# Optimization experiments

Hardware: AMD Instinct MI355X
Metric: run time of the kernel (lower is better)

Reference implementation:

```python
import jax, jax.numpy as jnp
import numpy as np
from jax import lax

N_IN = 512      # n_input == n_output of decoder
N_H = 2048      # n_hidden
N_L = 2         # n_layers (encoder/decoder GRU stacks written out explicitly)
SEQ = 2048      # sequence length
SPARSITY = 0.1  # sparsity_level -> k_sparse = int(N_H * SPARSITY)


def setup_inputs() -> dict:
    key = jax.random.key(0)
    ks = jax.random.split(key, 14)
    s = 0.02
    f32 = jnp.float32
    return {
        "sequence": jax.random.normal(ks[0], (SEQ, N_IN), f32),
        # encoder GRU (pytorch layout: W_ih [3H, in], W_hh [3H, H], gate order r,z,n)
        "enc_Wih0": jax.random.normal(ks[1], (3 * N_H, N_IN), f32) * s,
        "enc_Wih1": jax.random.normal(ks[2], (3 * N_H, N_H), f32) * s,
        "enc_Whh": jax.random.normal(ks[3], (N_L, 3 * N_H, N_H), f32) * s,
        "enc_bih": jax.random.normal(ks[4], (N_L, 3 * N_H), f32) * s,
        "enc_bhh": jax.random.normal(ks[5], (N_L, 3 * N_H), f32) * s,
        # decoder GRU (input dim = N_IN)
        "dec_Wih0": jax.random.normal(ks[6], (3 * N_H, N_IN), f32) * s,
        "dec_Wih1": jax.random.normal(ks[7], (3 * N_H, N_H), f32) * s,
        "dec_Whh": jax.random.normal(ks[8], (N_L, 3 * N_H, N_H), f32) * s,
        "dec_bih": jax.random.normal(ks[9], (N_L, 3 * N_H), f32) * s,
        "dec_bhh": jax.random.normal(ks[10], (N_L, 3 * N_H), f32) * s,
        # decoder output Linear: n_hidden -> n_output
        "dec_Wout": jax.random.normal(ks[11], (N_IN, N_H), f32) * s,
        "dec_bout": jax.random.normal(ks[12], (N_IN,), f32) * s,
    }


def _gru_cell(x, h, Wih, Whh, bih, bhh):
    # x: [in], h: [H]; PyTorch GRU equations, gate order (r, z, n)
    gi = Wih @ x + bih
    gh = Whh @ h + bhh
    ir, iz, inn = jnp.split(gi, 3)
    hr, hz, hn = jnp.split(gh, 3)
    r = jax.nn.sigmoid(ir + hr)
    z = jax.nn.sigmoid(iz + hz)
    n = jnp.tanh(inn + r * hn)
    return (1.0 - z) * n + z * h


def reference(sequence, enc_Wih0, enc_Wih1, enc_Whh, enc_bih, enc_bhh,
              dec_Wih0, dec_Wih1, dec_Whh, dec_bih, dec_bhh,
              dec_Wout, dec_bout):
    seq_len = sequence.shape[0]

    # ---- encoder: 2-layer GRU over the sequence, batch=1 (batch dim dropped) ----
    def enc_step(h, x):
        h0 = _gru_cell(x, h[0], enc_Wih0, enc_Whh[0], enc_bih[0], enc_bhh[0])
        h1 = _gru_cell(h0, h[1], enc_Wih1, enc_Whh[1], enc_bih[1], enc_bhh[1])
        return jnp.stack([h0, h1]), None

    h0_init = jnp.zeros((N_L, N_H), sequence.dtype)
    enc_hidden, _ = lax.scan(enc_step, h0_init, sequence)

    # ---- top-k sparsity on innermost (last) layer of the hidden state ----
    k_sparse = int(N_H * SPARSITY)
    h_last = enc_hidden[N_L - 1]
    _, top_idx = lax.top_k(h_last, k_sparse)
    mask = jnp.zeros((N_H,), h_last.dtype).at[top_idx].set(1.0)
    enc_hidden = enc_hidden.at[N_L - 1].set(h_last * mask)

    # ---- decoder: seq_len-1 single-step GRU+Linear, targets are sequence reversed ----
    targets = jnp.flip(sequence[: seq_len - 1], axis=0)  # sequence[seq_len-2-i]

    def dec_step(carry, target):
        x, h = carry
        h0 = _gru_cell(x, h[0], dec_Wih0, dec_Whh[0], dec_bih[0], dec_bhh[0])
        h1 = _gru_cell(h0, h[1], dec_Wih1, dec_Whh[1], dec_bih[1], dec_bhh[1])
        out = dec_Wout @ h1 + dec_bout
        step_loss = jnp.mean((out - target) ** 2)
        return (out, jnp.stack([h0, h1])), (out, step_loss)

    init = (sequence[seq_len - 1], enc_hidden)
    _, (reconstructed, step_losses) = lax.scan(dec_step, init, targets)
    loss = jnp.sum(step_losses) / seq_len
    return reconstructed, loss
```

## Files before the change

kernel.cpp:

```cpp
#include <hip/hip_runtime.h>
#include <hip/hip_cooperative_groups.h>

namespace cg = cooperative_groups;

#define H      2048
#define NIN    512
#define TH     (3 * H)
#define SEQLEN 2048
#define KSP    204
#define NBLK   256
#define NTHR   512
#define NWAVES (NBLK * (NTHR / 64))

static_assert(NWAVES == H, "one wave per hidden element");

struct Params {
    const float* seq;
    const float* eWih0; const float* eWih1; const float* eWhh;
    const float* ebih;  const float* ebhh;
    const float* dWih0; const float* dWih1; const float* dWhh;
    const float* dbih;  const float* dbhh;
    const float* dWout; const float* dbout;
    float* out;
    float* ws;
};

__device__ __forceinline__ float wave_reduce_f(float v) {
#pragma unroll
    for (int m = 32; m >= 1; m >>= 1) v += __shfl_xor(v, m, 64);
    return v;
}

template <int XDIM>
__device__ __forceinline__ void gru_phase(int j, int lane,
    const float* __restrict__ Wih, const float* __restrict__ Whh,
    const float* __restrict__ bih, const float* __restrict__ bhh,
    const float* __restrict__ x,
    const float* __restrict__ hcur, float* __restrict__ hnxt)
{
    const float4* wir = (const float4*)(Wih + (size_t)j * XDIM);
    const float4* wiz = (const float4*)(Wih + (size_t)(H + j) * XDIM);
    const float4* win = (const float4*)(Wih + (size_t)(2 * H + j) * XDIM);
    const float4* whr = (const float4*)(Whh + (size_t)j * H);
    const float4* whz = (const float4*)(Whh + (size_t)(H + j) * H);
    const float4* whn = (const float4*)(Whh + (size_t)(2 * H + j) * H);
    const float4* x4  = (const float4*)x;
    const float4* h4  = (const float4*)hcur;

    float air = 0.f, aiz = 0.f, ain = 0.f;
#pragma unroll
    for (int k = 0; k < XDIM / 256; ++k) {
        int i = lane + 64 * k;
        float4 xv = x4[i];
        float4 a = wir[i], b = wiz[i], c = win[i];
        air = fmaf(a.x, xv.x, air); air = fmaf(a.y, xv.y, air);
        air = fmaf(a.z, xv.z, air); air = fmaf(a.w, xv.w, air);
        aiz = fmaf(b.x, xv.x, aiz); aiz = fmaf(b.y, xv.y, aiz);
        aiz = fmaf(b.z, xv.z, aiz); aiz = fmaf(b.w, xv.w, aiz);
        ain = fmaf(c.x, xv.x, ain); ain = fmaf(c.y, xv.y, ain);
        ain = fmaf(c.z, xv.z, ain); ain = fmaf(c.w, xv.w, ain);
    }
    float ahr = 0.f, ahz = 0.f, ahn = 0.f;
#pragma unroll
    for (int k = 0; k < H / 256; ++k) {
        int i = lane + 64 * k;
        float4 hv = h4[i];
        float4 a = whr[i], b = whz[i], c = whn[i];
        ahr = fmaf(a.x, hv.x, ahr); ahr = fmaf(a.y, hv.y, ahr);
        ahr = fmaf(a.z, hv.z, ahr); ahr = fmaf(a.w, hv.w, ahr);
        ahz = fmaf(b.x, hv.x, ahz); ahz = fmaf(b.y, hv.y, ahz);
        ahz = fmaf(b.z, hv.z, ahz); ahz = fmaf(b.w, hv.w, ahz);
        ahn = fmaf(c.x, hv.x, ahn); ahn = fmaf(c.y, hv.y, ahn);
        ahn = fmaf(c.z, hv.z, ahn); ahn = fmaf(c.w, hv.w, ahn);
    }
    float sr   = wave_reduce_f(air + ahr);
    float sz   = wave_reduce_f(aiz + ahz);
    float sin_ = wave_reduce_f(ain);
    float shn  = wave_reduce_f(ahn);

    if (lane == 0) {
        float r = 1.f / (1.f + expf(-(sr + bih[j] + bhh[j])));
        float z = 1.f / (1.f + expf(-(sz + bih[H + j] + bhh[H + j])));
        float n = tanhf(sin_ + bih[2 * H + j] + r * (shn + bhh[2 * H + j]));
        hnxt[j] = (1.f - z) * n + z * hcur[j];
    }
}

__global__ void __launch_bounds__(NTHR)
seqae_kernel(Params p)
{
    cg::grid_group grid = cg::this_grid();
    const int lane = threadIdx.x & 63;
    const int wid  = blockIdx.x * (NTHR / 64) + (threadIdx.x >> 6);

    float* loss = p.ws;
    float* h0a  = p.ws + 64;
    float* h0b  = h0a + H;
    float* h1a  = h0b + H;
    float* h1b  = h1a + H;

    {
        int gtid = blockIdx.x * NTHR + threadIdx.x;
        if (gtid == 0) *loss = 0.f;
        for (int i = gtid; i < H; i += NBLK * NTHR) { h0a[i] = 0.f; h1a[i] = 0.f; }
    }
    grid.sync();

    const float* ebih0 = p.ebih;        const float* ebih1 = p.ebih + TH;
    const float* ebhh0 = p.ebhh;        const float* ebhh1 = p.ebhh + TH;
    const float* eWhh0 = p.eWhh;        const float* eWhh1 = p.eWhh + (size_t)TH * H;

    float* h0c = h0a; float* h0n = h0b;
    float* h1c = h1a; float* h1n = h1b;

    for (int t = 0; t < SEQLEN; ++t) {
        const float* x = p.seq + (size_t)t * NIN;
        gru_phase<NIN>(wid, lane, p.eWih0, eWhh0, ebih0, ebhh0, x, h0c, h0n);
        grid.sync();
        gru_phase<H>(wid, lane, p.eWih1, eWhh1, ebih1, ebhh1, h0n, h1c, h1n);
        grid.sync();
        float* tmp;
        tmp = h0c; h0c = h0n; h0n = tmp;
        tmp = h1c; h1c = h1n; h1n = tmp;
    }

    {
        int j = wid;
        float vj = h1c[j];
        int cnt = 0;
        for (int i = lane; i < H; i += 64) {
            float vi = h1c[i];
            cnt += (vi > vj) || (vi == vj && i < j);
        }
#pragma unroll
        for (int m = 32; m >= 1; m >>= 1) cnt += __shfl_xor(cnt, m, 64);
        if (lane == 0) h1n[j] = (cnt < KSP) ? vj : 0.f;
    }
    grid.sync();
    { float* tmp = h1c; h1c = h1n; h1n = tmp; }

    const float* dbih0 = p.dbih;        const float* dbih1 = p.dbih + TH;
    const float* dbhh0 = p.dbhh;        const float* dbhh1 = p.dbhh + TH;
    const float* dWhh0 = p.dWhh;        const float* dWhh1 = p.dWhh + (size_t)TH * H;

    float lsum = 0.f;
    for (int t = 0; t < SEQLEN - 1; ++t) {
        const float* x = (t == 0) ? (p.seq + (size_t)(SEQLEN - 1) * NIN)
                                  : (p.out + (size_t)(t - 1) * NIN);
        gru_phase<NIN>(wid, lane, p.dWih0, dWhh0, dbih0, dbhh0, x, h0c, h0n);
        grid.sync();
        gru_phase<H>(wid, lane, p.dWih1, dWhh1, dbih1, dbhh1, h0n, h1c, h1n);
        grid.sync();
        if (wid < NIN) {
            int j = wid;
            const float4* wo = (const float4*)(p.dWout + (size_t)j * H);
            const float4* h4 = (const float4*)h1n;
            float a = 0.f;
#pragma unroll
            for (int k = 0; k < H / 256; ++k) {
                int i = lane + 64 * k;
                float4 w = wo[i]; float4 hv = h4[i];
                a = fmaf(w.x, hv.x, a); a = fmaf(w.y, hv.y, a);
                a = fmaf(w.z, hv.z, a); a = fmaf(w.w, hv.w, a);
            }
            a = wave_reduce_f(a);
            if (lane == 0) {
                float o = a + p.dbout[j];
                p.out[(size_t)t * NIN + j] = o;
                float tg = p.seq[(size_t)(SEQLEN - 2 - t) * NIN + j];
                float d = o - tg;
                lsum = fmaf(d, d, lsum);
            }
        }
        grid.sync();
        float* tmp;
        tmp = h0c; h0c = h0n; h0n = tmp;
        tmp = h1c; h1c = h1n; h1n = tmp;
    }

    if (wid < NIN && lane == 0) atomicAdd(loss, lsum);
    grid.sync();
    if (blockIdx.x == 0 && threadIdx.x == 0) {
        p.out[(size_t)(SEQLEN - 1) * NIN] = (*loss) * (1.f / ((float)NIN * (float)SEQLEN));
    }
}

extern "C" void kernel_launch(void* const* d_in, const int* in_sizes, int n_in,
                              void* d_out, int out_size, void* d_ws, size_t ws_size,
                              hipStream_t stream)
{
    Params p;
    p.seq   = (const float*)d_in[0];
    p.eWih0 = (const float*)d_in[1];
    p.eWih1 = (const float*)d_in[2];
    p.eWhh  = (const float*)d_in[3];
    p.ebih  = (const float*)d_in[4];
    p.ebhh  = (const float*)d_in[5];
    p.dWih0 = (const float*)d_in[6];
    p.dWih1 = (const float*)d_in[7];
    p.dWhh  = (const float*)d_in[8];
    p.dbih  = (const float*)d_in[9];
    p.dbhh  = (const float*)d_in[10];
    p.dWout = (const float*)d_in[11];
    p.dbout = (const float*)d_in[12];
    p.out = (float*)d_out;
    p.ws  = (float*)d_ws;

    void* args[] = { &p };
    (void)hipLaunchCooperativeKernel((void*)seqae_kernel, dim3(NBLK), dim3(NTHR),
                                     args, 0, stream);
}
```

Measured before the change: 396.1 ms.

## Keep FP16-packed GRU weights resident in registers and pipeline encoder layers

Adds pack kernels that convert all GRU and output weights to fp16 in a lane-interleaved layout inside the workspace. The main cooperative kernel then keeps each wave's weight rows in registers for the whole encoder or decoder loop, so it no longer re-streams about 100MB of weights from memory every timestep. The encoder also skews layer 1 by one step so both layers run in the same phase, halving the grid syncs per step. The cost is fp16 rounding of the weights, very high register pressure (possible spills), and extra pack launches on every call. A fallback path is kept for when the workspace is too small.

```diff
diff --git a/kernel.cpp b/kernel.cpp
--- a/kernel.cpp
+++ b/kernel.cpp
@@ -1,4 +1,5 @@
 #include <hip/hip_runtime.h>
+#include <hip/hip_fp16.h>
 #include <hip/hip_cooperative_groups.h>
 
 namespace cg = cooperative_groups;
@@ -10,9 +11,20 @@
 #define KSP    204
 #define NBLK   256
 #define NTHR   512
-#define NWAVES (NBLK * (NTHR / 64))
-
-static_assert(NWAVES == H, "one wave per hidden element");
+
+typedef unsigned int uint32;
+
+constexpr long O_EA = 0;
+constexpr long O_EB = O_EA + 1572864;
+constexpr long O_EC = O_EB + 6291456;
+constexpr long O_ED = O_EC + 6291456;
+constexpr long O_DA = O_ED + 6291456;
+constexpr long O_DB = O_DA + 1572864;
+constexpr long O_DC = O_DB + 6291456;
+constexpr long O_DD = O_DC + 6291456;
+constexpr long O_WO = O_DD + 6291456;
+constexpr long U_TOTAL = O_WO + 524288;
+constexpr size_t WS_STATE_BYTES = 65536;
 
 struct Params {
     const float* seq;
@@ -31,8 +43,223 @@
     return v;
 }
 
+__device__ __forceinline__ float sigmoidf_(float v) { return 1.f / (1.f + expf(-v)); }
+
+__device__ __forceinline__ float2 h2f(uint32 u) {
+    __half2 h = *reinterpret_cast<__half2*>(&u);
+    return __half22float2(h);
+}
+
+__global__ void pack_kernel(const float* __restrict__ src, uint32* __restrict__ dst,
+                            int total, int xdim, int nrows)
+{
+    int KK = xdim / 256;
+    for (int i = blockIdx.x * blockDim.x + threadIdx.x; i < total;
+         i += gridDim.x * blockDim.x) {
+        int l = i & 63;
+        int rest = i >> 6;
+        int p2 = rest & 1; rest >>= 1;
+        int kk = rest % KK; rest /= KK;
+        int r  = rest % nrows; rest /= nrows;
+        int j  = rest;
+        int c0 = 256 * kk + 4 * l + 2 * p2;
+        const float* row = src + ((size_t)r * H + j) * xdim;
+        unsigned short b0 = __half_as_ushort(__float2half_rn(row[c0]));
+        unsigned short b1 = __half_as_ushort(__float2half_rn(row[c0 + 1]));
+        dst[i] = ((uint32)b1 << 16) | b0;
+    }
+}
+
+template <int NU>
+__device__ __forceinline__ void load_seg3(uint32 (&dst)[3][NU], const uint32* seg,
+                                          int j, int lane)
+{
+#pragma unroll
+    for (int r = 0; r < 3; ++r)
+#pragma unroll
+        for (int u = 0; u < NU; ++u)
+            dst[r][u] = seg[((size_t)(j * 3 + r) * NU + u) * 64 + lane];
+}
+
+__device__ __forceinline__ void load_seg1(uint32 (&dst)[16], const uint32* seg,
+                                          int j, int lane)
+{
+#pragma unroll
+    for (int u = 0; u < 16; ++u)
+        dst[u] = seg[((size_t)j * 16 + u) * 64 + lane];
+}
+
+template <int NU>
+__device__ __forceinline__ void dot3h(const uint32 (&w)[3][NU],
+                                      const float* __restrict__ vec, int lane,
+                                      float acc[3])
+{
+#pragma unroll
+    for (int kk = 0; kk < NU / 2; ++kk) {
+        float4 v = ((const float4*)vec)[kk * 64 + lane];
+#pragma unroll
+        for (int r = 0; r < 3; ++r) {
+            float2 lo = h2f(w[r][2 * kk]);
+            float2 hi = h2f(w[r][2 * kk + 1]);
+            acc[r] = fmaf(lo.x, v.x, acc[r]);
+            acc[r] = fmaf(lo.y, v.y, acc[r]);
+            acc[r] = fmaf(hi.x, v.z, acc[r]);
+            acc[r] = fmaf(hi.y, v.w, acc[r]);
+        }
+    }
+}
+
+template <int NUX>
+__device__ __forceinline__ float gru_cell_reg(int j, int lane,
+    const uint32 (&wi)[3][NUX], const uint32 (&wh)[3][16],
+    const float* __restrict__ x, const float* __restrict__ h,
+    float bir, float biz, float bin, float bhr, float bhz, float bhn)
+{
+    float ai[3] = {0.f, 0.f, 0.f}, ah[3] = {0.f, 0.f, 0.f};
+    dot3h<NUX>(wi, x, lane, ai);
+    dot3h<16>(wh, h, lane, ah);
+    float hj  = h[j];
+    float sr  = wave_reduce_f(ai[0] + ah[0]);
+    float sz  = wave_reduce_f(ai[1] + ah[1]);
+    float sn  = wave_reduce_f(ai[2]);
+    float shn = wave_reduce_f(ah[2]);
+    float r = sigmoidf_(sr + bir + bhr);
+    float z = sigmoidf_(sz + biz + bhz);
+    float n = tanhf(sn + bin + r * (shn + bhn));
+    return (1.f - z) * n + z * hj;
+}
+
+__global__ void __launch_bounds__(NTHR, 2)
+seqae_reg_kernel(Params p)
+{
+    cg::grid_group grid = cg::this_grid();
+    const int lane = threadIdx.x & 63;
+    const int j    = blockIdx.x * (NTHR / 64) + (threadIdx.x >> 6);
+
+    float* loss = p.ws;
+    float* h0b[2] = { p.ws + 64, p.ws + 64 + H };
+    float* h1b[2] = { p.ws + 64 + 2 * H, p.ws + 64 + 3 * H };
+    const uint32* U = (const uint32*)((const char*)p.ws + WS_STATE_BYTES);
+
+    {
+        int gtid = blockIdx.x * NTHR + threadIdx.x;
+        if (gtid == 0) *loss = 0.f;
+        for (int i = gtid; i < H; i += NBLK * NTHR) { h0b[0][i] = 0.f; h1b[0][i] = 0.f; }
+    }
+    grid.sync();
+
+    uint32 wa[3][4], wb[3][16], wc[3][16], wd[3][16];
+    load_seg3<4>(wa, U + O_EA, j, lane);
+    load_seg3<16>(wb, U + O_EB, j, lane);
+    load_seg3<16>(wc, U + O_EC, j, lane);
+    load_seg3<16>(wd, U + O_ED, j, lane);
+
+    float eb[12];
+    {
+        const float* bi0 = p.ebih;      const float* bi1 = p.ebih + TH;
+        const float* bh0 = p.ebhh;      const float* bh1 = p.ebhh + TH;
+        eb[0] = bi0[j]; eb[1] = bi0[H + j]; eb[2] = bi0[2 * H + j];
+        eb[3] = bh0[j]; eb[4] = bh0[H + j]; eb[5] = bh0[2 * H + j];
+        eb[6] = bi1[j]; eb[7] = bi1[H + j]; eb[8] = bi1[2 * H + j];
+        eb[9] = bh1[j]; eb[10] = bh1[H + j]; eb[11] = bh1[2 * H + j];
+    }
+
+    int c0 = 0, c1 = 0;
+
+    for (int ph = 0; ph <= SEQLEN; ++ph) {
+        const float* h0old = h0b[c0];
+        float h0v = 0.f, h1v = 0.f;
+        if (ph < SEQLEN)
+            h0v = gru_cell_reg<4>(j, lane, wa, wb, p.seq + (size_t)ph * NIN, h0old,
+                                  eb[0], eb[1], eb[2], eb[3], eb[4], eb[5]);
+        if (ph >= 1)
+            h1v = gru_cell_reg<16>(j, lane, wc, wd, h0old, h1b[c1],
+                                   eb[6], eb[7], eb[8], eb[9], eb[10], eb[11]);
+        if (lane == 0) {
+            if (ph < SEQLEN) h0b[c0 ^ 1][j] = h0v;
+            if (ph >= 1)     h1b[c1 ^ 1][j] = h1v;
+        }
+        grid.sync();
+        if (ph < SEQLEN) c0 ^= 1;
+        if (ph >= 1)     c1 ^= 1;
+    }
+
+    {
+        const float* hs = h1b[c1];
+        float vj = hs[j];
+        int cnt = 0;
+        for (int i = lane; i < H; i += 64) {
+            float vi = hs[i];
+            cnt += (vi > vj) || (vi == vj && i < j);
+        }
+#pragma unroll
+        for (int m = 32; m >= 1; m >>= 1) cnt += __shfl_xor(cnt, m, 64);
+        if (lane == 0) h1b[c1 ^ 1][j] = (cnt < KSP) ? vj : 0.f;
+    }
+    grid.sync();
+    c1 ^= 1;
+
+    load_seg3<4>(wa, U + O_DA, j, lane);
+    load_seg3<16>(wb, U + O_DB, j, lane);
+    load_seg3<16>(wc, U + O_DC, j, lane);
+    load_seg3<16>(wd, U + O_DD, j, lane);
+    uint32 wo[16];
+    load_seg1(wo, U + O_WO, j & (NIN - 1), lane);
+
+    float db[12], boutj;
+    {
+        const float* bi0 = p.dbih;      const float* bi1 = p.dbih + TH;
+        const float* bh0 = p.dbhh;      const float* bh1 = p.dbhh + TH;
+        db[0] = bi0[j]; db[1] = bi0[H + j]; db[2] = bi0[2 * H + j];
+        db[3] = bh0[j]; db[4] = bh0[H + j]; db[5] = bh0[2 * H + j];
+        db[6] = bi1[j]; db[7] = bi1[H + j]; db[8] = bi1[2 * H + j];
+        db[9] = bh1[j]; db[10] = bh1[H + j]; db[11] = bh1[2 * H + j];
+        boutj = p.dbout[j & (NIN - 1)];
+    }
+
+    float lsum = 0.f;
+    for (int t = 0; t < SEQLEN - 1; ++t) {
+        const float* x = (t == 0) ? (p.seq + (size_t)(SEQLEN - 1) * NIN)
+                                  : (p.out + (size_t)(t - 1) * NIN);
+        float h0v = gru_cell_reg<4>(j, lane, wa, wb, x, h0b[c0],
+                                    db[0], db[1], db[2], db[3], db[4], db[5]);
+        if (lane == 0) h0b[c0 ^ 1][j] = h0v;
+        grid.sync(); c0 ^= 1;
+
+        float h1v = gru_cell_reg<16>(j, lane, wc, wd, h0b[c0], h1b[c1],
+                                     db[6], db[7], db[8], db[9], db[10], db[11]);
+        if (lane == 0) h1b[c1 ^ 1][j] = h1v;
+        grid.sync(); c1 ^= 1;
+
+        if (j < NIN) {
+            const float* h1n = h1b[c1];
+            float a = 0.f;
+#pragma unroll
+            for (int kk = 0; kk < 8; ++kk) {
+                float4 v = ((const float4*)h1n)[kk * 64 + lane];
+                float2 lo = h2f(wo[2 * kk]);
+                float2 hi = h2f(wo[2 * kk + 1]);
+                a = fmaf(lo.x, v.x, a); a = fmaf(lo.y, v.y, a);
+                a = fmaf(hi.x, v.z, a); a = fmaf(hi.y, v.w, a);
+            }
+            a = wave_reduce_f(a);
+            float o = a + boutj;
+            if (lane == 0) p.out[(size_t)t * NIN + j] = o;
+            float tg = p.seq[(size_t)(SEQLEN - 2 - t) * NIN + j];
+            float d = o - tg;
+            lsum = fmaf(d, d, lsum);
+        }
+        grid.sync();
+    }
+
+    if (j < NIN && lane == 0) atomicAdd(loss, lsum);
+    grid.sync();
+    if (blockIdx.x == 0 && threadIdx.x == 0)
+        p.out[(size_t)(SEQLEN - 1) * NIN] = (*loss) * (1.f / ((float)NIN * (float)SEQLEN));
+}
+
 template <int XDIM>
-__device__ __forceinline__ void gru_phase(int j, int lane,
+__device__ __forceinline__ void gru_phase_fb(int j, int lane,
     const float* __restrict__ Wih, const float* __restrict__ Whh,
     const float* __restrict__ bih, const float* __restrict__ bhh,
     const float* __restrict__ x,
@@ -79,15 +306,15 @@
     float shn  = wave_reduce_f(ahn);
 
     if (lane == 0) {
-        float r = 1.f / (1.f + expf(-(sr + bih[j] + bhh[j])));
-        float z = 1.f / (1.f + expf(-(sz + bih[H + j] + bhh[H + j])));
+        float r = sigmoidf_(sr + bih[j] + bhh[j]);
+        float z = sigmoidf_(sz + bih[H + j] + bhh[H + j]);
         float n = tanhf(sin_ + bih[2 * H + j] + r * (shn + bhh[2 * H + j]));
         hnxt[j] = (1.f - z) * n + z * hcur[j];
     }
 }
 
 __global__ void __launch_bounds__(NTHR)
-seqae_kernel(Params p)
+seqae_fallback_kernel(Params p)
 {
     cg::grid_group grid = cg::this_grid();
     const int lane = threadIdx.x & 63;
@@ -115,9 +342,9 @@
 
     for (int t = 0; t < SEQLEN; ++t) {
         const float* x = p.seq + (size_t)t * NIN;
-        gru_phase<NIN>(wid, lane, p.eWih0, eWhh0, ebih0, ebhh0, x, h0c, h0n);
-        grid.sync();
-        gru_phase<H>(wid, lane, p.eWih1, eWhh1, ebih1, ebhh1, h0n, h1c, h1n);
+        gru_phase_fb<NIN>(wid, lane, p.eWih0, eWhh0, ebih0, ebhh0, x, h0c, h0n);
+        grid.sync();
+        gru_phase_fb<H>(wid, lane, p.eWih1, eWhh1, ebih1, ebhh1, h0n, h1c, h1n);
         grid.sync();
         float* tmp;
         tmp = h0c; h0c = h0n; h0n = tmp;
@@ -147,9 +374,9 @@
     for (int t = 0; t < SEQLEN - 1; ++t) {
         const float* x = (t == 0) ? (p.seq + (size_t)(SEQLEN - 1) * NIN)
                                   : (p.out + (size_t)(t - 1) * NIN);
-        gru_phase<NIN>(wid, lane, p.dWih0, dWhh0, dbih0, dbhh0, x, h0c, h0n);
-        grid.sync();
-        gru_phase<H>(wid, lane, p.dWih1, dWhh1, dbih1, dbhh1, h0n, h1c, h1n);
+        gru_phase_fb<NIN>(wid, lane, p.dWih0, dWhh0, dbih0, dbhh0, x, h0c, h0n);
+        grid.sync();
+        gru_phase_fb<H>(wid, lane, p.dWih1, dWhh1, dbih1, dbhh1, h0n, h1c, h1n);
         grid.sync();
         if (wid < NIN) {
             int j = wid;
@@ -206,7 +433,26 @@
     p.out = (float*)d_out;
     p.ws  = (float*)d_ws;
 
-    void* args[] = { &p };
-    (void)hipLaunchCooperativeKernel((void*)seqae_kernel, dim3(NBLK), dim3(NTHR),
-                                     args, 0, stream);
-}
+    size_t need = WS_STATE_BYTES + (size_t)U_TOTAL * 4;
+    if (ws_size >= need) {
+        uint32* U = (uint32*)((char*)d_ws + WS_STATE_BYTES);
+        const int PB = 256, PG = 1024;
+        pack_kernel<<<PG, PB, 0, stream>>>(p.eWih0, U + O_EA, 1572864, NIN, 3);
+        pack_kernel<<<PG, PB, 0, stream>>>(p.eWhh,  U + O_EB, 6291456, H, 3);
+        pack_kernel<<<PG, PB, 0, stream>>>(p.eWih1, U + O_EC, 6291456, H, 3);
+        pack_kernel<<<PG, PB, 0, stream>>>(p.eWhh + (size_t)TH * H, U + O_ED, 6291456, H, 3);
+        pack_kernel<<<PG, PB, 0, stream>>>(p.dWih0, U + O_DA, 1572864, NIN, 3);
+        pack_kernel<<<PG, PB, 0, stream>>>(p.dWhh,  U + O_DB, 6291456, H, 3);
+        pack_kernel<<<PG, PB, 0, stream>>>(p.dWih1, U + O_DC, 6291456, H, 3);
+        pack_kernel<<<PG, PB, 0, stream>>>(p.dWhh + (size_t)TH * H, U + O_DD, 6291456, H, 3);
+        pack_kernel<<<PG, PB, 0, stream>>>(p.dWout, U + O_WO, 524288, H, 1);
+
+        void* args[] = { &p };
+        (void)hipLaunchCooperativeKernel((void*)seqae_reg_kernel, dim3(NBLK), dim3(NTHR),
+                                         args, 0, stream);
+    } else {
+        void* args[] = { &p };
+        (void)hipLaunchCooperativeKernel((void*)seqae_fallback_kernel, dim3(NBLK), dim3(NTHR),
+                                         args, 0, stream);
+    }
+}
```

New measurement: 370.6 ms. -6.4%, faster.
